# Kernel optimization log

Hardware: AMD Instinct MI355X
Metric: run time of the kernel (lower is better)

The kernel has to match this reference:

```python
import jax, jax.numpy as jnp
import numpy as np

R_CUT = 2.5
N_BASIS = 8
BOX_SIZE = 10.0


def radial_encode(r, n, r_cut):
    """Gaussian radial basis on squared distance r: (...,) -> (..., n).
    Centers spread over [0, r_cut], width r_cut/n. (Helper source not given;
    this is the standard RBF encode used in such MD graph nets.)"""
    mu = jnp.linspace(0.0, r_cut, n, dtype=r.dtype)        # (n,)
    sigma = r_cut / n
    d = r[..., None] - mu                                   # (..., n)
    return jnp.exp(-0.5 * (d / sigma) ** 2)


def setup_inputs() -> dict:
    key = jax.random.key(0)
    k1, k2 = jax.random.split(key)
    batch, nodes, deg = 8, 20000, 32
    pos = jax.random.uniform(k1, (batch, nodes, 3), dtype=jnp.float32) * BOX_SIZE
    box = jnp.full((3,), BOX_SIZE, dtype=jnp.float32)
    nbr_idx = jax.random.randint(k2, (nodes, deg), 0, nodes, dtype=jnp.int64)
    return {"pos": pos, "box": box, "nbr_idx": nbr_idx}


def reference(pos, box, nbr_idx):
    # pos: (B, N, 3); box: (3,); nbr_idx: (N, deg)
    ang_box = box / (2.0 * jnp.pi)                          # (3,)
    # edges_read: gather neighbor positions -> (B, N, deg, 3)
    nbr_pos = pos[:, nbr_idx]                               # (B, N, deg, 3)
    edges = nbr_pos - pos[:, :, None]                       # relative displacement
    # periodic-box sin wrap
    edges = ang_box * jnp.sin(edges / ang_box)
    r = jnp.sum(edges ** 2, axis=-1)                        # (B, N, deg) squared dist
    x = radial_encode(r, N_BASIS, R_CUT)                    # (B, N, deg, 8)
    xv = x[..., None] * edges[..., None, :]                 # (B, N, deg, 8, 3) outer product
    # edges_reduce: sum over neighbor axis
    y = jnp.sum(x, axis=2)                                  # (B, N, 8)
    yv = jnp.sum(xv, axis=2)                                # (B, N, 8, 3)
    return (y, yv)
```

## Files before the change

kernel.cpp:

```cpp
#include <hip/hip_runtime.h>

static constexpr int BATCH = 8;
static constexpr int NODES = 20000;
static constexpr int DEG   = 32;
static constexpr int NB    = 8;

#if defined(__has_builtin) && __has_builtin(__builtin_amdgcn_exp2f)
#define EXP2F(x) __builtin_amdgcn_exp2f(x)
#else
#define EXP2F(x) exp2f(x)
#endif

typedef float float2v __attribute__((ext_vector_type(2)));
typedef float float4v __attribute__((ext_vector_type(4)));

static constexpr float C1 = -7.3865986f;
static constexpr float C2 = 5.2761417f;
static constexpr float H1 = 0.5204500f;
static constexpr float S0A = 0.0733695f;
static constexpr float S0B = 0.00538308f;
static constexpr float S1A = 3.94957e-4f;
static constexpr float S1B = 2.89776e-5f;
static constexpr float S2A = 2.12617e-6f;
static constexpr float S2B = 1.55990e-7f;

__global__ __launch_bounds__(256)
void transpose_pos_kernel(const float* __restrict__ pos, float4* __restrict__ pos_t) {
    const int t = blockIdx.x * blockDim.x + threadIdx.x;
    if (t >= BATCH * NODES) return;
    const int b = t / NODES;
    const int i = t - b * NODES;
    pos_t[(size_t)i * BATCH + b] =
        make_float4(pos[3 * t + 0], pos[3 * t + 1], pos[3 * t + 2], 0.0f);
}

__global__ __launch_bounds__(256, 4)
void graph_embed_kernel(const float4* __restrict__ pos_t,
                        const float* __restrict__ box,
                        const int*   __restrict__ nbr,
                        float* __restrict__ out)
{
    __shared__ float y_lds[8 * 132];
    __shared__ float yv_lds[8 * 388];

    const int tid = threadIdx.x;
    const int t   = blockIdx.x * 256 + tid;
    const int b   = t & 7;
    const int jh  = (t >> 3) & 1;
    const int i   = t >> 4;
    const int i_sub  = tid >> 4;
    const int i_base = blockIdx.x * 16;

    const float inv2pi = 0.15915494309189535f;
    const float ab0 = box[0] * inv2pi;
    const float ab1 = box[1] * inv2pi;
    const float ab2 = box[2] * inv2pi;
    const float ia0 = 1.0f / ab0;
    const float ia1 = 1.0f / ab1;
    const float ia2 = 1.0f / ab2;

    const float2v s0 = { S0A, S0B };
    const float2v s1 = { S1A, S1B };
    const float2v s2 = { S2A, S2B };

    const float4 p = pos_t[(size_t)i * BATCH + b];

    float2v yA[4], vA0[4], vA1[4], vA2[4];
#pragma unroll
    for (int pp = 0; pp < 4; ++pp) {
        yA[pp] = (float2v)0.f; vA0[pp] = (float2v)0.f;
        vA1[pp] = (float2v)0.f; vA2[pp] = (float2v)0.f;
    }

    const int4* __restrict__ row4 = (const int4*)(nbr + (size_t)i * DEG) + jh * 4;
    const int4 rr0 = row4[0], rr1 = row4[1], rr2 = row4[2], rr3 = row4[3];
    const int4 rr[4] = { rr0, rr1, rr2, rr3 };

    float4 q0 = pos_t[(size_t)rr[0].x * BATCH + b];
    float4 q1 = pos_t[(size_t)rr[0].y * BATCH + b];
    float4 q2 = pos_t[(size_t)rr[0].z * BATCH + b];
    float4 q3 = pos_t[(size_t)rr[0].w * BATCH + b];

#pragma unroll
    for (int g = 0; g < 4; ++g) {
        float4 n0, n1, n2, n3;
        if (g + 1 < 4) {
            const int4 nx = rr[g + 1];
            n0 = pos_t[(size_t)nx.x * BATCH + b];
            n1 = pos_t[(size_t)nx.y * BATCH + b];
            n2 = pos_t[(size_t)nx.z * BATCH + b];
            n3 = pos_t[(size_t)nx.w * BATCH + b];
        }
        const float4 qs[4] = { q0, q1, q2, q3 };
#pragma unroll
        for (int jj = 0; jj < 4; ++jj) {
            const float4 q = qs[jj];
            const float e0 = ab0 * __sinf((q.x - p.x) * ia0);
            const float e1 = ab1 * __sinf((q.y - p.y) * ia1);
            const float e2 = ab2 * __sinf((q.z - p.z) * ia2);
            const float r  = fmaf(e0, e0, fmaf(e1, e1, e2 * e2));

            const float gg  = EXP2F(r * C2);
            const float gg2 = gg * gg;
            const float x0  = EXP2F(r * r * C1);
            float2v xp = { x0, x0 * gg * H1 };
            const float2v m0 = gg2 * s0;
            const float2v m1 = gg2 * s1;
            const float2v m2 = gg2 * s2;

            yA[0] += xp; vA0[0] += xp * e0; vA1[0] += xp * e1; vA2[0] += xp * e2;
            xp *= m0;
            yA[1] += xp; vA0[1] += xp * e0; vA1[1] += xp * e1; vA2[1] += xp * e2;
            xp *= m1;
            yA[2] += xp; vA0[2] += xp * e0; vA1[2] += xp * e1; vA2[2] += xp * e2;
            xp *= m2;
            yA[3] += xp; vA0[3] += xp * e0; vA1[3] += xp * e1; vA2[3] += xp * e2;
        }
        q0 = n0; q1 = n1; q2 = n2; q3 = n3;
    }

#pragma unroll
    for (int pp = 0; pp < 4; ++pp) {
        yA[pp].x  += __shfl_xor(yA[pp].x, 8);  yA[pp].y  += __shfl_xor(yA[pp].y, 8);
        vA0[pp].x += __shfl_xor(vA0[pp].x, 8); vA0[pp].y += __shfl_xor(vA0[pp].y, 8);
        vA1[pp].x += __shfl_xor(vA1[pp].x, 8); vA1[pp].y += __shfl_xor(vA1[pp].y, 8);
        vA2[pp].x += __shfl_xor(vA2[pp].x, 8); vA2[pp].y += __shfl_xor(vA2[pp].y, 8);
    }

    if ((tid & 8) == 0) {
        float* yl = y_lds + b * 132 + i_sub * 8;
        float* vl = yv_lds + b * 388 + i_sub * 24;
#pragma unroll
        for (int pp = 0; pp < 4; ++pp) {
            yl[2 * pp]     = yA[pp].x;
            yl[2 * pp + 1] = yA[pp].y;
            vl[6 * pp + 0] = vA0[pp].x;
            vl[6 * pp + 1] = vA1[pp].x;
            vl[6 * pp + 2] = vA2[pp].x;
            vl[6 * pp + 3] = vA0[pp].y;
            vl[6 * pp + 4] = vA1[pp].y;
            vl[6 * pp + 5] = vA2[pp].y;
        }
    }
    __syncthreads();

    {
        const int bb  = tid >> 5;
        const int off = tid & 31;
        float4v* dst = (float4v*)(out + (size_t)(bb * NODES + i_base) * NB + off * 4);
        const float4v val = *(const float4v*)(y_lds + bb * 132 + off * 4);
        __builtin_nontemporal_store(val, dst);
    }
    float* __restrict__ outv = out + (size_t)BATCH * NODES * NB;
#pragma unroll
    for (int s = 0; s < 3; ++s) {
        const int idx = tid + s * 256;
        const int bb  = idx / 96;
        const int rem = idx - bb * 96;
        float4v* dst = (float4v*)(outv + (size_t)(bb * NODES + i_base) * (NB * 3) + rem * 4);
        const float4v val = *(const float4v*)(yv_lds + bb * 388 + rem * 4);
        __builtin_nontemporal_store(val, dst);
    }
}

__global__ __launch_bounds__(256)
void graph_embed_fallback_kernel(const float* __restrict__ pos,
                                 const float* __restrict__ box,
                                 const int*   __restrict__ nbr,
                                 float* __restrict__ out)
{
    const int t = blockIdx.x * blockDim.x + threadIdx.x;
    if (t >= BATCH * NODES) return;
    const int b = t / NODES;
    const int i = t - b * NODES;

    const float inv2pi = 0.15915494309189535f;
    const float ab0 = box[0] * inv2pi, ab1 = box[1] * inv2pi, ab2 = box[2] * inv2pi;
    const float ia0 = 1.0f / ab0, ia1 = 1.0f / ab1, ia2 = 1.0f / ab2;

    float h[NB - 1];
#pragma unroll
    for (int k = 0; k < NB - 1; ++k)
        h[k] = __expf(-0.6530612245f * (float)(2 * k + 1));

    const float* __restrict__ pb = pos + (size_t)b * NODES * 3;
    const float p0 = pb[3 * i + 0], p1 = pb[3 * i + 1], p2 = pb[3 * i + 2];

    float y0[NB], v0[NB], v1[NB], v2[NB];
#pragma unroll
    for (int k = 0; k < NB; ++k) { y0[k] = 0.f; v0[k] = 0.f; v1[k] = 0.f; v2[k] = 0.f; }

    const int* __restrict__ row = nbr + (size_t)i * DEG;
#pragma unroll 4
    for (int j = 0; j < DEG; ++j) {
        const int idx = row[j];
        const float* __restrict__ q = pb + (size_t)idx * 3;
        const float e0 = ab0 * __sinf((q[0] - p0) * ia0);
        const float e1 = ab1 * __sinf((q[1] - p1) * ia1);
        const float e2 = ab2 * __sinf((q[2] - p2) * ia2);
        const float r  = fmaf(e0, e0, fmaf(e1, e1, e2 * e2));
        const float g = EXP2F(r * C2);
        float x = EXP2F(r * r * C1);
#pragma unroll
        for (int k = 0; k < NB; ++k) {
            y0[k] += x;
            v0[k] = fmaf(x, e0, v0[k]);
            v1[k] = fmaf(x, e1, v1[k]);
            v2[k] = fmaf(x, e2, v2[k]);
            if (k < NB - 1) x = x * g * h[k];
        }
    }

    float* __restrict__ yptr = out + (size_t)t * NB;
    *(float4*)(yptr + 0) = make_float4(y0[0], y0[1], y0[2], y0[3]);
    *(float4*)(yptr + 4) = make_float4(y0[4], y0[5], y0[6], y0[7]);
    float* __restrict__ vptr = out + (size_t)BATCH * NODES * NB + (size_t)t * (NB * 3);
    *(float4*)(vptr +  0) = make_float4(v0[0], v1[0], v2[0], v0[1]);
    *(float4*)(vptr +  4) = make_float4(v1[1], v2[1], v0[2], v1[2]);
    *(float4*)(vptr +  8) = make_float4(v2[2], v0[3], v1[3], v2[3]);
    *(float4*)(vptr + 12) = make_float4(v0[4], v1[4], v2[4], v0[5]);
    *(float4*)(vptr + 16) = make_float4(v1[5], v2[5], v0[6], v1[6]);
    *(float4*)(vptr + 20) = make_float4(v2[6], v0[7], v1[7], v2[7]);
}

extern "C" void kernel_launch(void* const* d_in, const int* in_sizes, int n_in,
                              void* d_out, int out_size, void* d_ws, size_t ws_size,
                              hipStream_t stream) {
    const float* pos = (const float*)d_in[0];
    const float* box = (const float*)d_in[1];
    const int*   nbr = (const int*)d_in[2];
    float* out = (float*)d_out;

    const int total = BATCH * NODES;
    const size_t packed_bytes = (size_t)total * sizeof(float4);
    const int block = 256;
    if (ws_size >= packed_bytes) {
        float4* pos_t = (float4*)d_ws;
        transpose_pos_kernel<<<(total + block - 1) / block, block, 0, stream>>>(pos, pos_t);
        graph_embed_kernel<<<(total * 2) / block, block, 0, stream>>>(pos_t, box, nbr, out);
    } else {
        graph_embed_fallback_kernel<<<(total + block - 1) / block, block, 0, stream>>>(pos, box, nbr, out);
    }
}
```

Measured before the change: 80.69 us.

## Split neighbor loop across four threads per node and stage transpose via LDS

The embed kernel now assigns four threads per (node, batch) pair, each handling 8 neighbors instead of 16, and adds a second xor-shuffle reduction level. Blocks cover 8 nodes, doubling grid size, to raise parallelism and memory-level concurrency for the random gathers. Neighbor indices are read with nontemporal loads. The transpose kernel is rewritten to do coalesced reads of pos into LDS and then write the interleaved float4 layout, avoiding strided global reads. The cost is more shuffle work and more redundant per-thread setup per node.

```diff
diff --git a/kernel.cpp b/kernel.cpp
--- a/kernel.cpp
+++ b/kernel.cpp
@@ -13,6 +13,7 @@
 
 typedef float float2v __attribute__((ext_vector_type(2)));
 typedef float float4v __attribute__((ext_vector_type(4)));
+typedef int   int4v   __attribute__((ext_vector_type(4)));
 
 static constexpr float C1 = -7.3865986f;
 static constexpr float C2 = 5.2761417f;
@@ -26,12 +27,26 @@
 
 __global__ __launch_bounds__(256)
 void transpose_pos_kernel(const float* __restrict__ pos, float4* __restrict__ pos_t) {
-    const int t = blockIdx.x * blockDim.x + threadIdx.x;
-    if (t >= BATCH * NODES) return;
-    const int b = t / NODES;
-    const int i = t - b * NODES;
-    pos_t[(size_t)i * BATCH + b] =
-        make_float4(pos[3 * t + 0], pos[3 * t + 1], pos[3 * t + 2], 0.0f);
+    __shared__ float p_lds[8 * 97];
+    const int tid    = threadIdx.x;
+    const int i_base = blockIdx.x * 32;
+
+#pragma unroll
+    for (int s = 0; s < 3; ++s) {
+        const int idx = tid + s * 256;
+        const int seg = idx / 96;
+        const int off = idx - seg * 96;
+        p_lds[seg * 97 + off] =
+            pos[(size_t)seg * NODES * 3 + (size_t)i_base * 3 + off];
+    }
+    __syncthreads();
+
+    const int i_sub = tid >> 3;
+    const int b     = tid & 7;
+    const float x = p_lds[b * 97 + i_sub * 3 + 0];
+    const float y = p_lds[b * 97 + i_sub * 3 + 1];
+    const float z = p_lds[b * 97 + i_sub * 3 + 2];
+    pos_t[(size_t)(i_base + i_sub) * BATCH + b] = make_float4(x, y, z, 0.0f);
 }
 
 __global__ __launch_bounds__(256, 4)
@@ -40,16 +55,16 @@
                         const int*   __restrict__ nbr,
                         float* __restrict__ out)
 {
-    __shared__ float y_lds[8 * 132];
-    __shared__ float yv_lds[8 * 388];
+    __shared__ float y_lds[8 * 68];
+    __shared__ float yv_lds[8 * 196];
 
     const int tid = threadIdx.x;
     const int t   = blockIdx.x * 256 + tid;
     const int b   = t & 7;
-    const int jh  = (t >> 3) & 1;
-    const int i   = t >> 4;
-    const int i_sub  = tid >> 4;
-    const int i_base = blockIdx.x * 16;
+    const int jq  = (t >> 3) & 3;
+    const int i   = t >> 5;
+    const int i_sub  = tid >> 5;
+    const int i_base = blockIdx.x * 8;
 
     const float inv2pi = 0.15915494309189535f;
     const float ab0 = box[0] * inv2pi;
@@ -72,24 +87,23 @@
         vA1[pp] = (float2v)0.f; vA2[pp] = (float2v)0.f;
     }
 
-    const int4* __restrict__ row4 = (const int4*)(nbr + (size_t)i * DEG) + jh * 4;
-    const int4 rr0 = row4[0], rr1 = row4[1], rr2 = row4[2], rr3 = row4[3];
-    const int4 rr[4] = { rr0, rr1, rr2, rr3 };
-
-    float4 q0 = pos_t[(size_t)rr[0].x * BATCH + b];
-    float4 q1 = pos_t[(size_t)rr[0].y * BATCH + b];
-    float4 q2 = pos_t[(size_t)rr[0].z * BATCH + b];
-    float4 q3 = pos_t[(size_t)rr[0].w * BATCH + b];
-
-#pragma unroll
-    for (int g = 0; g < 4; ++g) {
+    const int4v* __restrict__ row4 = (const int4v*)(nbr + (size_t)i * DEG) + jq * 2;
+    const int4v rr0 = __builtin_nontemporal_load(row4);
+    const int4v rr1 = __builtin_nontemporal_load(row4 + 1);
+
+    float4 q0 = pos_t[(size_t)rr0.x * BATCH + b];
+    float4 q1 = pos_t[(size_t)rr0.y * BATCH + b];
+    float4 q2 = pos_t[(size_t)rr0.z * BATCH + b];
+    float4 q3 = pos_t[(size_t)rr0.w * BATCH + b];
+
+#pragma unroll
+    for (int g = 0; g < 2; ++g) {
         float4 n0, n1, n2, n3;
-        if (g + 1 < 4) {
-            const int4 nx = rr[g + 1];
-            n0 = pos_t[(size_t)nx.x * BATCH + b];
-            n1 = pos_t[(size_t)nx.y * BATCH + b];
-            n2 = pos_t[(size_t)nx.z * BATCH + b];
-            n3 = pos_t[(size_t)nx.w * BATCH + b];
+        if (g == 0) {
+            n0 = pos_t[(size_t)rr1.x * BATCH + b];
+            n1 = pos_t[(size_t)rr1.y * BATCH + b];
+            n2 = pos_t[(size_t)rr1.z * BATCH + b];
+            n3 = pos_t[(size_t)rr1.w * BATCH + b];
         }
         const float4 qs[4] = { q0, q1, q2, q3 };
 #pragma unroll
@@ -126,10 +140,17 @@
         vA1[pp].x += __shfl_xor(vA1[pp].x, 8); vA1[pp].y += __shfl_xor(vA1[pp].y, 8);
         vA2[pp].x += __shfl_xor(vA2[pp].x, 8); vA2[pp].y += __shfl_xor(vA2[pp].y, 8);
     }
-
-    if ((tid & 8) == 0) {
-        float* yl = y_lds + b * 132 + i_sub * 8;
-        float* vl = yv_lds + b * 388 + i_sub * 24;
+#pragma unroll
+    for (int pp = 0; pp < 4; ++pp) {
+        yA[pp].x  += __shfl_xor(yA[pp].x, 16);  yA[pp].y  += __shfl_xor(yA[pp].y, 16);
+        vA0[pp].x += __shfl_xor(vA0[pp].x, 16); vA0[pp].y += __shfl_xor(vA0[pp].y, 16);
+        vA1[pp].x += __shfl_xor(vA1[pp].x, 16); vA1[pp].y += __shfl_xor(vA1[pp].y, 16);
+        vA2[pp].x += __shfl_xor(vA2[pp].x, 16); vA2[pp].y += __shfl_xor(vA2[pp].y, 16);
+    }
+
+    if ((tid & 24) == 0) {
+        float* yl = y_lds + b * 68 + i_sub * 8;
+        float* vl = yv_lds + b * 196 + i_sub * 24;
 #pragma unroll
         for (int pp = 0; pp < 4; ++pp) {
             yl[2 * pp]     = yA[pp].x;
@@ -144,22 +165,25 @@
     }
     __syncthreads();
 
-    {
-        const int bb  = tid >> 5;
-        const int off = tid & 31;
+    if (tid < 128) {
+        const int bb  = tid >> 4;
+        const int off = tid & 15;
         float4v* dst = (float4v*)(out + (size_t)(bb * NODES + i_base) * NB + off * 4);
-        const float4v val = *(const float4v*)(y_lds + bb * 132 + off * 4);
+        const float4v val = *(const float4v*)(y_lds + bb * 68 + off * 4);
         __builtin_nontemporal_store(val, dst);
     }
     float* __restrict__ outv = out + (size_t)BATCH * NODES * NB;
 #pragma unroll
-    for (int s = 0; s < 3; ++s) {
+    for (int s = 0; s < 2; ++s) {
         const int idx = tid + s * 256;
-        const int bb  = idx / 96;
-        const int rem = idx - bb * 96;
-        float4v* dst = (float4v*)(outv + (size_t)(bb * NODES + i_base) * (NB * 3) + rem * 4);
-        const float4v val = *(const float4v*)(yv_lds + bb * 388 + rem * 4);
-        __builtin_nontemporal_store(val, dst);
+        if (idx < 384) {
+            const int bb  = idx / 48;
+            const int rem = idx - bb * 48;
+            float4v* dst =
+                (float4v*)(outv + (size_t)(bb * NODES + i_base) * (NB * 3) + rem * 4);
+            const float4v val = *(const float4v*)(yv_lds + bb * 196 + rem * 4);
+            __builtin_nontemporal_store(val, dst);
+        }
     }
 }
 
@@ -236,8 +260,8 @@
     const int block = 256;
     if (ws_size >= packed_bytes) {
         float4* pos_t = (float4*)d_ws;
-        transpose_pos_kernel<<<(total + block - 1) / block, block, 0, stream>>>(pos, pos_t);
-        graph_embed_kernel<<<(total * 2) / block, block, 0, stream>>>(pos_t, box, nbr, out);
+        transpose_pos_kernel<<<NODES / 32, block, 0, stream>>>(pos, pos_t);
+        graph_embed_kernel<<<(total * 4) / block, block, 0, stream>>>(pos_t, box, nbr, out);
     } else {
         graph_embed_fallback_kernel<<<(total + block - 1) / block, block, 0, stream>>>(pos, box, nbr, out);
     }
```

Measured after the change: 82.88 us. +2.7%, slower.
